# Kernel tuning notes

Measured on AMD Instinct MI355X. Metric: run time of the kernel, lower is better.

Reference implementation:

```python
import jax, jax.numpy as jnp
import numpy as np

B, T, D, H = 2, 2048, 512, 8
HD = D // H


def _mha(x, Wi, bi, Wo, bo):
    # torch nn.MultiheadAttention with q=k=v=x, eval mode (no dropout), batch-first math
    b, t, d = x.shape
    qkv = x @ Wi.T + bi                      # (b,t,3D)
    q, k, v = jnp.split(qkv, 3, axis=-1)
    q = q.reshape(b, t, H, HD)
    k = k.reshape(b, t, H, HD)
    v = v.reshape(b, t, H, HD)
    scores = jnp.einsum('bqhd,bkhd->bhqk', q, k) / jnp.sqrt(jnp.float32(HD))
    attn = jax.nn.softmax(scores, axis=-1)   # (b,H,t,t)
    out = jnp.einsum('bhqk,bkhd->bqhd', attn, v).reshape(b, t, d) @ Wo.T + bo
    return out, attn.mean(axis=1)            # weights averaged over heads, torch default


def _block_ids(t, c):
    # importance score is the constant c at every position (grad of sum == ones)
    cum = jnp.cumsum(jnp.full((t,), c, dtype=jnp.float32))
    frac = cum % 1.0
    boundary = (frac < jnp.roll(frac, 1)).astype(jnp.int32)
    return jnp.cumsum(boundary)              # ids in [0, max_blocks]


def _merge(x, ids, m):
    # segment-mean over dynamic blocks; block id 0 (pre-first-boundary) is dropped, as in torch loop i=1..max
    xm = jnp.moveaxis(x, 1, 0)               # (t,b,d)
    sums = jax.ops.segment_sum(xm, ids, num_segments=m + 1)[1:]              # (m,b,d)
    counts = jax.ops.segment_sum(jnp.ones(ids.shape[0], jnp.float32), ids, num_segments=m + 1)[1:]
    merged = sums / (counts[:, None, None] + 1e-10)
    return jnp.moveaxis(merged, 0, 1), counts


def setup_inputs():
    key = jax.random.key(0)
    ks = jax.random.split(key, 12)
    s = 0.02
    d = {'x': jax.random.normal(ks[0], (B, T, D), jnp.float32)}
    for i, n in enumerate(['char', 'block', 'glob']):
        d[n + '_Wi'] = jax.random.normal(ks[1 + 3 * i], (3 * D, D), jnp.float32) * s
        d[n + '_bi'] = jnp.zeros((3 * D,), jnp.float32)
        d[n + '_Wo'] = jax.random.normal(ks[2 + 3 * i], (D, D), jnp.float32) * s
        d[n + '_bo'] = jnp.zeros((D,), jnp.float32)
    d['merge_w'] = jax.random.normal(ks[10], (D,), jnp.float32) * 0.01
    d['merge_b'] = jnp.array([0.37], jnp.float32)
    d['gmerge_w'] = jax.random.normal(ks[11], (D,), jnp.float32) * 0.01
    d['gmerge_b'] = jnp.array([0.41], jnp.float32)
    return d


def reference(x, char_Wi, char_bi, char_Wo, char_bo, block_Wi, block_bi, block_Wo, block_bo,
              glob_Wi, glob_bi, glob_Wo, glob_bo, merge_w, merge_b, gmerge_w, gmerge_b):
    char_out, char_w = _mha(x, char_Wi, char_bi, char_Wo, char_bo)
    c1 = merge_w.sum() + merge_b[0]
    ids1 = _block_ids(T, c1)
    m1 = int(ids1.max())                      # data-independent given weights; concrete in eager
    blocks, cnt1 = _merge(char_out, ids1, m1)
    block_out, block_w = _mha(blocks, block_Wi, block_bi, block_Wo, block_bo)
    c2 = gmerge_w.sum() + gmerge_b[0]
    ids2 = _block_ids(m1, c2)
    m2 = int(ids2.max())
    glob, cnt2 = _merge(block_out, ids2, m2)
    glob_out, glob_w = _mha(glob, glob_Wi, glob_bi, glob_Wo, glob_bo)
    # double repeat_interleave expansion == gather: token t -> char block -> global block
    ids1n = np.asarray(ids1)
    ids2n = np.asarray(ids2)
    token_g = np.where(ids1n >= 1, ids2n[np.maximum(ids1n - 1, 0)], 0)
    tok_idx = np.nonzero(token_g >= 1)[0]
    expanded = glob_out[:, jnp.asarray(token_g[tok_idx] - 1), :]
    return expanded, char_w, block_w, glob_w
```

## Files before the change

kernel.cpp:

```cpp
#include <hip/hip_runtime.h>
#include <cstdint>
#include <cstddef>


#define TB 2
#define TT 2048
#define TD 512
#define TH 8
#define THD 64
#define KC 4

#define MI_M1 0
#define MI_M2 1
#define MI_NTOK 2
#define MI_OFF_CW 3
#define MI_OFF_BW 4
#define MI_OFF_GW 5
#define MI_MCHAR 6
#define MI_MBLOCK 7
#define MI_MGLOB 8
#define MI_SEQC 9
#define MI_SEQB 10
#define MI_SEQG 11

typedef _Float16 half8 __attribute__((ext_vector_type(8)));
typedef _Float16 half4 __attribute__((ext_vector_type(4)));
typedef _Float16 half2_t __attribute__((ext_vector_type(2)));
typedef float floatx4 __attribute__((ext_vector_type(4)));

__device__ __forceinline__ floatx4 mfma16(half8 a, half8 b, floatx4 c) {
  return __builtin_amdgcn_mfma_f32_16x16x32_f16(a, b, c, 0, 0, 0);
}
__device__ __forceinline__ floatx4 mfma16k16(half4 a, half4 b, floatx4 c) {
  return __builtin_amdgcn_mfma_f32_16x16x16f16(a, b, c, 0, 0, 0);
}

__device__ __forceinline__ void barrier_nodrain() {
  asm volatile("s_waitcnt lgkmcnt(0)" ::: "memory");
  __builtin_amdgcn_s_barrier();
}

__device__ __forceinline__ double fracd(double x) { return x - floor(x); }

__device__ int scan_phase(int n, double c, int* __restrict__ ids,
                          int* __restrict__ startg, float* __restrict__ cntg,
                          int* __restrict__ wsum, int t)
{
  int loc[8];
  const int base = t * 8;
#pragma unroll
  for (int j = 0; j < 8; ++j) {
    const int i = base + j;
    int f = 0;
    if (i < n) {
      const int pidx = (i == 0) ? n : i;
      f = (fracd((double)(i + 1) * c) < fracd((double)pidx * c)) ? 1 : 0;
    }
    loc[j] = f + ((j > 0) ? loc[j - 1] : 0);
  }
  wsum[t] = loc[7];
  __syncthreads();
  for (int off = 1; off < 256; off <<= 1) {
    int u = 0;
    if (t >= off) u = wsum[t - off];
    __syncthreads();
    wsum[t] += u;
    __syncthreads();
  }
  const int excl = wsum[t] - loc[7];
  const int m = wsum[255];
#pragma unroll
  for (int j = 0; j < 8; ++j) {
    const int i = base + j;
    if (i < n) {
      const int id = excl + loc[j];
      ids[i] = id;
      const int f = loc[j] - ((j > 0) ? loc[j - 1] : 0);
      if (f) startg[id - 1] = i;
    }
  }
  __syncthreads();
  for (int j = t; j < m; j += 256)
    cntg[j] = (float)((((j + 1) < m) ? startg[j + 1] : n) - startg[j]);
  __syncthreads();
  return m;
}

__global__ __launch_bounds__(256)
void meta_kernel(const float* __restrict__ mw, const float* __restrict__ mb,
                 const float* __restrict__ gw, const float* __restrict__ gb,
                 int* __restrict__ mi,
                 int* __restrict__ start1, float* __restrict__ cnt1,
                 int* __restrict__ start2, float* __restrict__ cnt2,
                 int* __restrict__ gmap)
{
  __shared__ int ids1[TT];
  __shared__ int ids2[TT];
  __shared__ int wsum[256];
  __shared__ double dsh[256];
  const int t = threadIdx.x;

  double s1 = 0.0, s2 = 0.0;
  for (int i = t; i < TD; i += 256) { s1 += (double)mw[i]; s2 += (double)gw[i]; }
  dsh[t] = s1; __syncthreads();
  for (int off = 128; off > 0; off >>= 1) {
    if (t < off) dsh[t] += dsh[t + off];
    __syncthreads();
  }
  const double c1 = dsh[0] + (double)mb[0];
  __syncthreads();
  dsh[t] = s2; __syncthreads();
  for (int off = 128; off > 0; off >>= 1) {
    if (t < off) dsh[t] += dsh[t + off];
    __syncthreads();
  }
  const double c2 = dsh[0] + (double)gb[0];
  __syncthreads();

  const int m1 = scan_phase(TT, c1, ids1, start1, cnt1, wsum, t);
  const int m2 = scan_phase(m1, c2, ids2, start2, cnt2, wsum, t);

  int i0 = TT;
  if (m1 >= 1 && m2 >= 1) i0 = start1[start2[0]];
  const int ntok = TT - i0;

  if (t == 0) {
    mi[MI_M1] = m1; mi[MI_M2] = m2; mi[MI_NTOK] = ntok;
    const int offcw = TB * ntok * TD;
    mi[MI_OFF_CW] = offcw;
    mi[MI_OFF_BW] = offcw + TB * TT * TT;
    mi[MI_OFF_GW] = offcw + TB * TT * TT + TB * m1 * m1;
    mi[MI_MCHAR] = TB * TT;
    mi[MI_MBLOCK] = TB * m1;
    mi[MI_MGLOB] = TB * m2;
    mi[MI_SEQC] = TT;
    mi[MI_SEQB] = m1;
    mi[MI_SEQG] = m2;
  }
  for (int i = i0 + t; i < TT; i += 256)
    gmap[i - i0] = ids2[ids1[i] - 1] - 1;
}

__global__ __launch_bounds__(256)
void prep_convert(const float* __restrict__ x,
                  const float* __restrict__ wi0, const float* __restrict__ wi1,
                  const float* __restrict__ wi2,
                  const float* __restrict__ wo0, const float* __restrict__ wo1,
                  const float* __restrict__ wo2,
                  _Float16* __restrict__ xh, _Float16* __restrict__ wiH,
                  _Float16* __restrict__ woH, _Float16* __restrict__ woL)
{
  const int r = blockIdx.y;
  const float* src;
  _Float16* dh;
  _Float16* dl = nullptr;
  int n;
  if (r == 0)      { src = x;   dh = xh;                              n = TB * TT * TD; }
  else if (r == 1) { src = wi0; dh = wiH;                             n = 3 * TD * TD; }
  else if (r == 2) { src = wi1; dh = wiH + (size_t)1 * 3 * TD * TD;   n = 3 * TD * TD; }
  else if (r == 3) { src = wi2; dh = wiH + (size_t)2 * 3 * TD * TD;   n = 3 * TD * TD; }
  else if (r == 4) { src = wo0; dh = woH; dl = woL;                   n = TD * TD; }
  else if (r == 5) { src = wo1; dh = woH + (size_t)TD * TD; dl = woL + (size_t)TD * TD; n = TD * TD; }
  else             { src = wo2; dh = woH + (size_t)2 * TD * TD; dl = woL + (size_t)2 * TD * TD; n = TD * TD; }

  const int stride = gridDim.x * 256 * 4;
  for (int i = (blockIdx.x * 256 + threadIdx.x) * 4; i < n; i += stride) {
    const float4 v = *(const float4*)&src[i];
    const float a[4] = {v.x, v.y, v.z, v.w};
    half4 h, l;
#pragma unroll
    for (int e = 0; e < 4; ++e) {
      const _Float16 hh = (_Float16)a[e];
      h[e] = hh;
      l[e] = (_Float16)(a[e] - (float)hh);
    }
    *(half4*)&dh[i] = h;
    if (dl) *(half4*)&dl[i] = l;
  }
}

__global__ __launch_bounds__(256)
void gemm_mfma(const _Float16* __restrict__ A, const _Float16* __restrict__ W,
               const float* __restrict__ bias, _Float16* __restrict__ C,
               const int* __restrict__ mi, int m_slot, int N)
{
  const int M = mi[m_slot];
  const int bm = blockIdx.y * 128;
  if (bm >= M) return;
  const int bn = blockIdx.x * 64;
  __shared__ _Float16 Ah[2][128][40];
  __shared__ _Float16 Wh[2][64][40];

  const int t = threadIdx.x;
  const int wv = t >> 6;
  const int lane = t & 63;
  const int l15 = lane & 15;
  const int quad = lane >> 4;
  const int srowA = t >> 1;
  const int ssegA = (t & 1) * 16;
  const int srowW = t >> 2;
  const int ssegW = (t & 3) * 8;
  const int ar = bm + srowA;
  const size_t abase = (size_t)ar * TD + ssegA;
  const size_t wbase = (size_t)(bn + srowW) * TD + ssegW;

  floatx4 acc[2][4];
#pragma unroll
  for (int i = 0; i < 2; ++i)
#pragma unroll
    for (int j = 0; j < 4; ++j) acc[i][j] = (floatx4){0.f, 0.f, 0.f, 0.f};

  const half8 h8z = {};
  half8 pa0, pa1, pw;

  auto LOADT = [&](int kk) {
    pa0 = h8z; pa1 = h8z;
    if (ar < M) {
      pa0 = *(const half8*)&A[abase + kk];
      pa1 = *(const half8*)&A[abase + kk + 8];
    }
    pw = *(const half8*)&W[wbase + kk];
  };
  auto WRITET = [&](int buf) {
    *(half8*)&Ah[buf][srowA][ssegA] = pa0;
    *(half8*)&Ah[buf][srowA][ssegA + 8] = pa1;
    *(half8*)&Wh[buf][srowW][ssegW] = pw;
  };

  LOADT(0);
  for (int it = 0; it < TD / 32; ++it) {
    const int buf = it & 1;
    WRITET(buf);
    if (it + 1 < TD / 32) LOADT((it + 1) * 32);
    barrier_nodrain();
    half8 ah[2];
#pragma unroll
    for (int mp = 0; mp < 2; ++mp)
      ah[mp] = *(const half8*)&Ah[buf][wv * 32 + mp * 16 + l15][quad * 8];
#pragma unroll
    for (int np = 0; np < 4; ++np) {
      const half8 bh = *(const half8*)&Wh[buf][np * 16 + l15][quad * 8];
#pragma unroll
      for (int mp = 0; mp < 2; ++mp)
        acc[mp][np] = mfma16(ah[mp], bh, acc[mp][np]);
    }
  }
  float bv[4];
#pragma unroll
  for (int np = 0; np < 4; ++np) bv[np] = bias[bn + np * 16 + l15];
#pragma unroll
  for (int mp = 0; mp < 2; ++mp) {
#pragma unroll
    for (int r = 0; r < 4; ++r) {
      const int row = bm + wv * 32 + mp * 16 + quad * 4 + r;
      if (row < M) {
        _Float16* cp = &C[(size_t)row * N + bn];
#pragma unroll
        for (int np = 0; np < 4; ++np)
          cp[np * 16 + l15] = (_Float16)(acc[mp][np][r] + bv[np]);
      }
    }
  }
}

__global__ __launch_bounds__(256)
void gemm_norm_mfma(const _Float16* __restrict__ Ob, const float* __restrict__ lb,
                    const _Float16* __restrict__ Whg, const _Float16* __restrict__ Wlg,
                    const float* __restrict__ bias,
                    float* __restrict__ C, const int* __restrict__ mi,
                    int m_slot, int seq_slot)
{
  const int M = mi[m_slot];
  const int bm = blockIdx.y * 64;
  if (bm >= M) return;
  const int seq = mi[seq_slot];
  const int bn = blockIdx.x * 64;
  __shared__ _Float16 Ah[2][64][40];
  __shared__ _Float16 Al[2][64][40];
  __shared__ _Float16 Wh[2][64][40];
  __shared__ _Float16 Wl[2][64][40];

  const int t = threadIdx.x;
  const int wv = t >> 6;
  const int lane = t & 63;
  const int l15 = lane & 15;
  const int quad = lane >> 4;
  const int srow = t >> 2;
  const int sseg = (t & 3) * 8;

  const int ar = bm + srow;
  const int ab = (ar >= seq) ? 1 : 0;
  const int aq = ar - ab * seq;
  const size_t wbase = (size_t)(bn + srow) * TD + sseg;

  floatx4 acc[4];
#pragma unroll
  for (int j = 0; j < 4; ++j) acc[j] = (floatx4){0.f, 0.f, 0.f, 0.f};

  const half8 h8z = {};
  half8 pOb[KC];
  float plb[KC];
  half8 pwh, pwl;

  auto LOADT = [&](int kk) {
    if (ar < M) {
      const size_t off = (size_t)ar * TD + kk + sseg;
#pragma unroll
      for (int z = 0; z < KC; ++z)
        pOb[z] = *(const half8*)&Ob[(size_t)z * 2097152 + off];
      const int h = kk >> 6;
      const size_t lidx = ((size_t)(ab * TH + h)) * 2048 + aq;
#pragma unroll
      for (int z = 0; z < KC; ++z) plb[z] = lb[(size_t)z * 32768 + lidx];
    } else {
#pragma unroll
      for (int z = 0; z < KC; ++z) { pOb[z] = h8z; plb[z] = 1.f; }
    }
    pwh = *(const half8*)&Whg[wbase + kk];
    pwl = *(const half8*)&Wlg[wbase + kk];
  };
  auto WRITET = [&](int buf) {
    float aa[8] = {0.f, 0.f, 0.f, 0.f, 0.f, 0.f, 0.f, 0.f};
    if (ar < M) {
#pragma unroll
      for (int z = 0; z < KC; ++z)
#pragma unroll
        for (int e = 0; e < 8; ++e) aa[e] += (float)pOb[z][e];
      const float lt = plb[0] + plb[1] + plb[2] + plb[3];
      const float linv = 1.f / lt;
#pragma unroll
      for (int e = 0; e < 8; ++e) aa[e] *= linv;
    }
    half8 hi, lo;
#pragma unroll
    for (int e = 0; e < 8; ++e) {
      const _Float16 h = (_Float16)aa[e];
      hi[e] = h; lo[e] = (_Float16)(aa[e] - (float)h);
    }
    *(half8*)&Ah[buf][srow][sseg] = hi;
    *(half8*)&Al[buf][srow][sseg] = lo;
    *(half8*)&Wh[buf][srow][sseg] = pwh;
    *(half8*)&Wl[buf][srow][sseg] = pwl;
  };

  LOADT(0);
  for (int it = 0; it < TD / 32; ++it) {
    const int buf = it & 1;
    WRITET(buf);
    if (it + 1 < TD / 32) LOADT((it + 1) * 32);
    barrier_nodrain();
    const half8 ah = *(const half8*)&Ah[buf][wv * 16 + l15][quad * 8];
    const half8 al = *(const half8*)&Al[buf][wv * 16 + l15][quad * 8];
#pragma unroll
    for (int np = 0; np < 4; ++np) {
      const half8 bh = *(const half8*)&Wh[buf][np * 16 + l15][quad * 8];
      const half8 bl = *(const half8*)&Wl[buf][np * 16 + l15][quad * 8];
      acc[np] = mfma16(al, bh, acc[np]);
      acc[np] = mfma16(ah, bl, acc[np]);
      acc[np] = mfma16(ah, bh, acc[np]);
    }
  }
  float bv[4];
#pragma unroll
  for (int np = 0; np < 4; ++np) bv[np] = bias[bn + np * 16 + l15];
#pragma unroll
  for (int r = 0; r < 4; ++r) {
    const int row = bm + wv * 16 + quad * 4 + r;
    if (row < M) {
      float* cp = &C[(size_t)row * 512 + bn];
#pragma unroll
      for (int np = 0; np < 4; ++np)
        cp[np * 16 + l15] = acc[np][r] + bv[np];
    }
  }
}

__global__ __launch_bounds__(256)
void attn1_mfma(const _Float16* __restrict__ qkv,
                float* __restrict__ lbase, _Float16* __restrict__ Obase,
                const int* __restrict__ mi, int seq_slot)
{
  const int seq = mi[seq_slot];
  const int q0 = blockIdx.x * 128;
  if (q0 >= seq) return;
  const int b = blockIdx.y >> 3, h = blockIdx.y & 7;
  const int z = blockIdx.z;
  float* lP = lbase + (size_t)z * 32768;
  _Float16* oP = Obase + (size_t)z * 2097152;
  const int t = threadIdx.x;
  const int wv = t >> 6;
  const int lane = t & 63;
  const int l15 = lane & 15;
  const int quad = lane >> 4;

  __shared__ __align__(16) char smem_raw[36864];
  float (*Ot)[68] = (float (*)[68])smem_raw;

  half8 qB[2][2];
#pragma unroll
  for (int mp = 0; mp < 2; ++mp) {
    const int qrow = q0 + wv * 32 + mp * 16 + l15;
#pragma unroll
    for (int c = 0; c < 2; ++c) {
      half8 v = {};
      if (qrow < seq)
        v = *(const half8*)&qkv[((size_t)(b * seq + qrow)) * 1536 + h * 64 + c * 32 + quad * 8];
      qB[mp][c] = v;
    }
  }
  half4 onesA;
#pragma unroll
  for (int j = 0; j < 4; ++j) onesA[j] = (_Float16)1.0f;

  floatx4 oacc[2][4];
#pragma unroll
  for (int i = 0; i < 2; ++i)
#pragma unroll
    for (int j = 0; j < 4; ++j) oacc[i][j] = (floatx4){0.f, 0.f, 0.f, 0.f};
  floatx4 lacc[2] = {(floatx4){0.f, 0.f, 0.f, 0.f}, (floatx4){0.f, 0.f, 0.f, 0.f}};

  const int nkt = (seq + 63) >> 6;
  const int nkc = (nkt + KC - 1) / KC;
  const int kt_beg = z * nkc;
  const int kt_end = min(kt_beg + nkc, nkt);

  const int krow = t >> 2;
  const int kseg = (t & 3) * 16;
  const int tp = lane & 31;
  const int dsel = lane >> 5;
  const int dbase = wv * 16 + dsel * 8;

  const half8 h8z = {};
  half8 pk0, pk1, pva, pvb;

  auto LOADKV = [&](int kt) {
    const int k0 = kt * 64;
    pk0 = h8z; pk1 = h8z; pva = h8z; pvb = h8z;
    const int kg = k0 + krow;
    if (kg < seq) {
      const _Float16* base = &qkv[((size_t)(b * seq + kg)) * 1536 + 512 + h * 64 + kseg];
      pk0 = *(const half8*)base;
      pk1 = *(const half8*)(base + 8);
    }
    const int kg0 = k0 + tp * 2;
    if (kg0 < seq)
      pva = *(const half8*)&qkv[((size_t)(b * seq + kg0)) * 1536 + 1024 + h * 64 + dbase];
    if (kg0 + 1 < seq)
      pvb = *(const half8*)&qkv[((size_t)(b * seq + kg0 + 1)) * 1536 + 1024 + h * 64 + dbase];
  };

  LOADKV(kt_beg);
  for (int kt = kt_beg; kt < kt_end; ++kt) {
    char* sb = smem_raw + (size_t)((kt - kt_beg) & 1) * 18432;
    _Float16 (*Kf)[72] = (_Float16 (*)[72])sb;
    _Float16 (*Vt)[72] = (_Float16 (*)[72])(sb + 9216);

    *(half8*)&Kf[krow][kseg] = pk0;
    *(half8*)&Kf[krow][kseg + 8] = pk1;
#pragma unroll
    for (int j = 0; j < 8; ++j) {
      half2_t pkk; pkk[0] = pva[j]; pkk[1] = pvb[j];
      *(half2_t*)&Vt[dbase + j][tp * 2] = pkk;
    }
    if (kt + 1 < kt_end) LOADKV(kt + 1);
    barrier_nodrain();

    const int k0 = kt * 64;
    const bool kfull = (k0 + 64 <= seq);
#pragma unroll
    for (int p = 0; p < 4; ++p) {
      floatx4 sT[2] = {(floatx4){0.f, 0.f, 0.f, 0.f}, (floatx4){0.f, 0.f, 0.f, 0.f}};
#pragma unroll
      for (int c = 0; c < 2; ++c) {
        const half8 kA = *(const half8*)&Kf[p * 16 + l15][c * 32 + quad * 8];
#pragma unroll
        for (int mp = 0; mp < 2; ++mp)
          sT[mp] = mfma16(kA, qB[mp][c], sT[mp]);
      }
      half4 vA[4];
#pragma unroll
      for (int dblk = 0; dblk < 4; ++dblk)
        vA[dblk] = *(const half4*)&Vt[dblk * 16 + l15][p * 16 + quad * 4];
      const int kg = k0 + p * 16 + quad * 4;
#pragma unroll
      for (int mp = 0; mp < 2; ++mp) {
        half4 eB;
        if (kfull) {
#pragma unroll
          for (int r = 0; r < 4; ++r)
            eB[r] = (_Float16)__expf(sT[mp][r] * 0.125f);
        } else {
#pragma unroll
          for (int r = 0; r < 4; ++r) {
            const float e = (kg + r < seq) ? __expf(sT[mp][r] * 0.125f) : 0.f;
            eB[r] = (_Float16)e;
          }
        }
        lacc[mp] = mfma16k16(onesA, eB, lacc[mp]);
#pragma unroll
        for (int dblk = 0; dblk < 4; ++dblk)
          oacc[mp][dblk] = mfma16k16(vA[dblk], eB, oacc[mp][dblk]);
      }
    }
  }

  __syncthreads();

#pragma unroll
  for (int mp = 0; mp < 2; ++mp) {
#pragma unroll
    for (int dblk = 0; dblk < 4; ++dblk)
      *(floatx4*)&Ot[wv * 16 + l15][dblk * 16 + quad * 4] = oacc[mp][dblk];
    const int ql = lane >> 2;
    const int dseg = (lane & 3) * 4;
    const int qg = q0 + wv * 32 + mp * 16 + ql;
    if (qg < seq) {
      _Float16* op = &oP[((size_t)(b * seq + qg)) * 512 + h * 64];
#pragma unroll
      for (int u = 0; u < 4; ++u) {
        const float4 v = *(const float4*)&Ot[wv * 16 + ql][u * 16 + dseg];
        half4 hv;
        hv[0] = (_Float16)v.x; hv[1] = (_Float16)v.y;
        hv[2] = (_Float16)v.z; hv[3] = (_Float16)v.w;
        *(half4*)(op + u * 16 + dseg) = hv;
      }
    }
    if (quad == 0) {
      const int qg2 = q0 + wv * 32 + mp * 16 + l15;
      if (qg2 < seq)
        lP[((size_t)(b * TH + h)) * 2048 + qg2] = lacc[mp][0];
    }
  }
}

__global__ __launch_bounds__(256)
void attn2_mfma(const _Float16* __restrict__ qkv,
                const float* __restrict__ lb,
                float* __restrict__ outb, const int* __restrict__ mi,
                int seq_slot, int off_slot)
{
  const int seq = mi[seq_slot];
  const int q0 = blockIdx.y * 64;
  const int k0 = blockIdx.x * 128;
  if (q0 >= seq || k0 >= seq) return;
  const int b = blockIdx.z;
  const int woff = mi[off_slot];
  float* wout = outb + (size_t)woff + (size_t)b * seq * seq;

  __shared__ _Float16 Ksh[2][128][72];
  __shared__ float Linv8[TH][64];

  const int t = threadIdx.x;
  const int wv = t >> 6;
  const int lane = t & 63;
  const int l15 = lane & 15;
  const int quad = lane >> 4;
  const int srowK = t >> 1;
  const int ssegK = (t & 1) * 32;

  for (int i = t; i < TH * 64; i += 256) {
    const int hh = i >> 6;
    const int qq = i & 63;
    float lv = 1.f;
    if (q0 + qq < seq) {
      const size_t lidx = ((size_t)(b * TH + hh)) * 2048 + q0 + qq;
      float lt = 0.f;
#pragma unroll
      for (int zz = 0; zz < KC; ++zz) lt += lb[(size_t)zz * 32768 + lidx];
      lv = lt;
    }
    Linv8[hh][qq] = 1.f / lv;
  }

  floatx4 acc[8];
#pragma unroll
  for (int j = 0; j < 8; ++j) acc[j] = (floatx4){0.f, 0.f, 0.f, 0.f};

  const int qr = q0 + wv * 16 + l15;
  const int kr = k0 + srowK;
  const bool qok = (qr < seq);
  const bool kok = (kr < seq);
  const size_t qoff = (size_t)(b * seq + qr) * 1536 + quad * 8;
  const size_t koff = (size_t)(b * seq + kr) * 1536 + 512 + ssegK;

  const half8 h8z = {};
  half8 pk[4];
  half8 qcur0, qcur1, qnxt0, qnxt1;

  auto LOADK = [&](int h) {
#pragma unroll
    for (int u = 0; u < 4; ++u) {
      pk[u] = h8z;
      if (kok) pk[u] = *(const half8*)&qkv[koff + h * 64 + u * 8];
    }
  };
  auto LOADQ = [&](int h, half8& d0, half8& d1) {
    d0 = h8z; d1 = h8z;
    if (qok) {
      d0 = *(const half8*)&qkv[qoff + h * 64];
      d1 = *(const half8*)&qkv[qoff + h * 64 + 32];
    }
  };

  LOADK(0);
  LOADQ(0, qcur0, qcur1);
  for (int h = 0; h < TH; ++h) {
    const int buf = h & 1;
#pragma unroll
    for (int u = 0; u < 4; ++u)
      *(half8*)&Ksh[buf][srowK][ssegK + u * 8] = pk[u];
    if (h + 1 < TH) { LOADK(h + 1); LOADQ(h + 1, qnxt0, qnxt1); }
    barrier_nodrain();

    float lv[4];
#pragma unroll
    for (int r = 0; r < 4; ++r)
      lv[r] = Linv8[h][wv * 16 + quad * 4 + r];

#pragma unroll
    for (int np = 0; np < 8; ++np) {
      const half8 bf0 = *(const half8*)&Ksh[buf][np * 16 + l15][quad * 8];
      const half8 bf1 = *(const half8*)&Ksh[buf][np * 16 + l15][32 + quad * 8];
      floatx4 s = (floatx4){0.f, 0.f, 0.f, 0.f};
      s = mfma16(qcur0, bf0, s);
      s = mfma16(qcur1, bf1, s);
#pragma unroll
      for (int r = 0; r < 4; ++r)
        acc[np][r] += __expf(s[r] * 0.125f) * lv[r];
    }
    qcur0 = qnxt0; qcur1 = qnxt1;
  }

#pragma unroll
  for (int r = 0; r < 4; ++r) {
    const int qg = q0 + wv * 16 + quad * 4 + r;
    if (qg >= seq) continue;
    float* rowp = wout + (size_t)qg * seq;
#pragma unroll
    for (int np = 0; np < 8; ++np) {
      const int col = k0 + np * 16 + l15;
      if (col < seq) rowp[col] = acc[np][r] * 0.125f;
    }
  }
}

__global__ __launch_bounds__(256)
void merge_kernel(const float* __restrict__ src, _Float16* __restrict__ dst,
                  const int* __restrict__ start, const float* __restrict__ cnt,
                  const int* __restrict__ mi, int seqin_slot, int seqout_slot)
{
  const int j = blockIdx.x;
  const int b = blockIdx.y;
  const int seqo = mi[seqout_slot];
  if (j >= seqo) return;
  const int seqi = mi[seqin_slot];
  const int s = start[j];
  const float cf = cnt[j];
  const int n = (int)cf;
  const int d0 = threadIdx.x * 2;
  float s0 = 0.f, s1 = 0.f;
  const float* p = &src[((size_t)b * seqi + s) * TD + d0];
  for (int i = 0; i < n; ++i) {
    const float2 v = *(const float2*)p;
    s0 += v.x; s1 += v.y;
    p += TD;
  }
  const float inv = 1.f / (cf + 1e-10f);
  half2_t o;
  o[0] = (_Float16)(s0 * inv);
  o[1] = (_Float16)(s1 * inv);
  *(half2_t*)&dst[((size_t)b * seqo + j) * TD + d0] = o;
}

__global__ __launch_bounds__(256)
void expand_kernel(const float* __restrict__ gout, float* __restrict__ dout,
                   const int* __restrict__ gmap, const int* __restrict__ mi)
{
  const int j = blockIdx.x;
  const int b = blockIdx.y;
  const int ntok = mi[MI_NTOK];
  if (j >= ntok) return;
  const int m2 = mi[MI_M2];
  const int g = gmap[j];
  const int d0 = threadIdx.x * 2;
  const float2 v = *(const float2*)&gout[((size_t)b * m2 + g) * TD + d0];
  *(float2*)&dout[((size_t)b * ntok + j) * TD + d0] = v;
}

extern "C" void kernel_launch(void* const* d_in, const int* in_sizes, int n_in,
                              void* d_out, int out_size, void* d_ws, size_t ws_size,
                              hipStream_t stream)
{
  const float* x   = (const float*)d_in[0];
  const float* cWi = (const float*)d_in[1];
  const float* cbi = (const float*)d_in[2];
  const float* cWo = (const float*)d_in[3];
  const float* cbo = (const float*)d_in[4];
  const float* bWi = (const float*)d_in[5];
  const float* bbi = (const float*)d_in[6];
  const float* bWo = (const float*)d_in[7];
  const float* bbo = (const float*)d_in[8];
  const float* gWi = (const float*)d_in[9];
  const float* gbi = (const float*)d_in[10];
  const float* gWo = (const float*)d_in[11];
  const float* gbo = (const float*)d_in[12];
  const float* mw  = (const float*)d_in[13];
  const float* mbv = (const float*)d_in[14];
  const float* gw  = (const float*)d_in[15];
  const float* gbv = (const float*)d_in[16];
  float* outf = (float*)d_out;

  char* wsb = (char*)d_ws;
  int*   mi     = (int*)(wsb);
  int*   start1 = (int*)(wsb + 1024);
  float* cnt1   = (float*)(wsb + 1024 + 8192);
  int*   start2 = (int*)(wsb + 1024 + 2 * 8192);
  float* cnt2   = (float*)(wsb + 1024 + 3 * 8192);
  int*   gmap   = (int*)(wsb + 1024 + 4 * 8192);
  float* lbase  = (float*)(wsb + 65536);
  _Float16* qkv = (_Float16*)(wsb + 655360);
  _Float16* Obase = (_Float16*)(wsb + 655360 + 12582912);
  float* stg_o  = (float*)(wsb + 30015488);
  _Float16* stg_mh = (_Float16*)(wsb + 38404096);
  _Float16* xh  = (_Float16*)(wsb + 42598400);
  _Float16* wiH = (_Float16*)(wsb + 46792704);
  _Float16* woH = (_Float16*)(wsb + 51511296);
  _Float16* woL = (_Float16*)(wsb + 53084160);

  const dim3 blk(256);

  meta_kernel<<<dim3(1), blk, 0, stream>>>(mw, mbv, gw, gbv, mi, start1, cnt1, start2, cnt2, gmap);
  prep_convert<<<dim3(256, 7), blk, 0, stream>>>(x, cWi, bWi, gWi, cWo, bWo, gWo,
                                                 xh, wiH, woH, woL);

  gemm_mfma<<<dim3(24, 32), blk, 0, stream>>>(xh, wiH, cbi, qkv, mi, MI_MCHAR, 1536);
  attn1_mfma<<<dim3(16, 16, KC), blk, 0, stream>>>(qkv, lbase, Obase, mi, MI_SEQC);
  attn2_mfma<<<dim3(16, 32, 2), blk, 0, stream>>>(qkv, lbase, outf, mi, MI_SEQC, MI_OFF_CW);
  gemm_norm_mfma<<<dim3(8, 64), blk, 0, stream>>>(Obase, lbase, woH, woL, cbo, stg_o, mi, MI_MCHAR, MI_SEQC);
  merge_kernel<<<dim3(2048, 2), blk, 0, stream>>>(stg_o, stg_mh, start1, cnt1, mi, MI_SEQC, MI_SEQB);

  gemm_mfma<<<dim3(24, 32), blk, 0, stream>>>(stg_mh, wiH + (size_t)786432, bbi, qkv, mi, MI_MBLOCK, 1536);
  attn1_mfma<<<dim3(16, 16, KC), blk, 0, stream>>>(qkv, lbase, Obase, mi, MI_SEQB);
  attn2_mfma<<<dim3(16, 32, 2), blk, 0, stream>>>(qkv, lbase, outf, mi, MI_SEQB, MI_OFF_BW);
  gemm_norm_mfma<<<dim3(8, 64), blk, 0, stream>>>(Obase, lbase, woH + (size_t)262144, woL + (size_t)262144, bbo, stg_o, mi, MI_MBLOCK, MI_SEQB);
  merge_kernel<<<dim3(2048, 2), blk, 0, stream>>>(stg_o, stg_mh, start2, cnt2, mi, MI_SEQB, MI_SEQG);

  gemm_mfma<<<dim3(24, 32), blk, 0, stream>>>(stg_mh, wiH + (size_t)2 * 786432, gbi, qkv, mi, MI_MGLOB, 1536);
  attn1_mfma<<<dim3(16, 16, KC), blk, 0, stream>>>(qkv, lbase, Obase, mi, MI_SEQG);
  attn2_mfma<<<dim3(16, 32, 2), blk, 0, stream>>>(qkv, lbase, outf, mi, MI_SEQG, MI_OFF_GW);
  gemm_norm_mfma<<<dim3(8, 64), blk, 0, stream>>>(Obase, lbase, woH + (size_t)2 * 262144, woL + (size_t)2 * 262144, gbo, stg_o, mi, MI_MGLOB, MI_SEQG);
  expand_kernel<<<dim3(2048, 2), blk, 0, stream>>>(stg_o, outf, gmap, mi);

  (void)in_sizes; (void)n_in; (void)out_size; (void)ws_size;
}
```

Measured before the change: 332.8 us.

## Fuse meta and prep kernels; double query tile in both attention passes

Merges the single-block metadata scan into the weight/input fp16 conversion launch as an extra grid row, saving one launch and letting the scan overlap the conversion. Doubles the query rows per block in attn1 (128 to 256) and attn2 (64 to 128), so each loaded K/V tile is reused across more queries with fewer blocks launched. The larger per-thread accumulators raise register pressure and halve the block count, which can lower occupancy and parallelism for the short block/global sequences.

```diff
diff --git a/kernel.cpp b/kernel.cpp
--- a/kernel.cpp
+++ b/kernel.cpp
@@ -87,12 +87,19 @@
 }
 
 __global__ __launch_bounds__(256)
-void meta_kernel(const float* __restrict__ mw, const float* __restrict__ mb,
-                 const float* __restrict__ gw, const float* __restrict__ gb,
-                 int* __restrict__ mi,
-                 int* __restrict__ start1, float* __restrict__ cnt1,
-                 int* __restrict__ start2, float* __restrict__ cnt2,
-                 int* __restrict__ gmap)
+void meta_prep(const float* __restrict__ mw, const float* __restrict__ mb,
+               const float* __restrict__ gw, const float* __restrict__ gb,
+               int* __restrict__ mi,
+               int* __restrict__ start1, float* __restrict__ cnt1,
+               int* __restrict__ start2, float* __restrict__ cnt2,
+               int* __restrict__ gmap,
+               const float* __restrict__ x,
+               const float* __restrict__ wi0, const float* __restrict__ wi1,
+               const float* __restrict__ wi2,
+               const float* __restrict__ wo0, const float* __restrict__ wo1,
+               const float* __restrict__ wo2,
+               _Float16* __restrict__ xh, _Float16* __restrict__ wiH,
+               _Float16* __restrict__ woH, _Float16* __restrict__ woL)
 {
   __shared__ int ids1[TT];
   __shared__ int ids2[TT];
@@ -100,56 +107,50 @@
   __shared__ double dsh[256];
   const int t = threadIdx.x;
 
-  double s1 = 0.0, s2 = 0.0;
-  for (int i = t; i < TD; i += 256) { s1 += (double)mw[i]; s2 += (double)gw[i]; }
-  dsh[t] = s1; __syncthreads();
-  for (int off = 128; off > 0; off >>= 1) {
-    if (t < off) dsh[t] += dsh[t + off];
+  if (blockIdx.y == 7) {
+    if (blockIdx.x != 0) return;
+    double s1 = 0.0, s2 = 0.0;
+    for (int i = t; i < TD; i += 256) { s1 += (double)mw[i]; s2 += (double)gw[i]; }
+    dsh[t] = s1; __syncthreads();
+    for (int off = 128; off > 0; off >>= 1) {
+      if (t < off) dsh[t] += dsh[t + off];
+      __syncthreads();
+    }
+    const double c1 = dsh[0] + (double)mb[0];
     __syncthreads();
-  }
-  const double c1 = dsh[0] + (double)mb[0];
-  __syncthreads();
-  dsh[t] = s2; __syncthreads();
-  for (int off = 128; off > 0; off >>= 1) {
-    if (t < off) dsh[t] += dsh[t + off];
+    dsh[t] = s2; __syncthreads();
+    for (int off = 128; off > 0; off >>= 1) {
+      if (t < off) dsh[t] += dsh[t + off];
+      __syncthreads();
+    }
+    const double c2 = dsh[0] + (double)gb[0];
     __syncthreads();
-  }
-  const double c2 = dsh[0] + (double)gb[0];
-  __syncthreads();
-
-  const int m1 = scan_phase(TT, c1, ids1, start1, cnt1, wsum, t);
-  const int m2 = scan_phase(m1, c2, ids2, start2, cnt2, wsum, t);
-
-  int i0 = TT;
-  if (m1 >= 1 && m2 >= 1) i0 = start1[start2[0]];
-  const int ntok = TT - i0;
-
-  if (t == 0) {
-    mi[MI_M1] = m1; mi[MI_M2] = m2; mi[MI_NTOK] = ntok;
-    const int offcw = TB * ntok * TD;
-    mi[MI_OFF_CW] = offcw;
-    mi[MI_OFF_BW] = offcw + TB * TT * TT;
-    mi[MI_OFF_GW] = offcw + TB * TT * TT + TB * m1 * m1;
-    mi[MI_MCHAR] = TB * TT;
-    mi[MI_MBLOCK] = TB * m1;
-    mi[MI_MGLOB] = TB * m2;
-    mi[MI_SEQC] = TT;
-    mi[MI_SEQB] = m1;
-    mi[MI_SEQG] = m2;
-  }
-  for (int i = i0 + t; i < TT; i += 256)
-    gmap[i - i0] = ids2[ids1[i] - 1] - 1;
-}
-
-__global__ __launch_bounds__(256)
-void prep_convert(const float* __restrict__ x,
-                  const float* __restrict__ wi0, const float* __restrict__ wi1,
-                  const float* __restrict__ wi2,
-                  const float* __restrict__ wo0, const float* __restrict__ wo1,
-                  const float* __restrict__ wo2,
-                  _Float16* __restrict__ xh, _Float16* __restrict__ wiH,
-                  _Float16* __restrict__ woH, _Float16* __restrict__ woL)
-{
+
+    const int m1 = scan_phase(TT, c1, ids1, start1, cnt1, wsum, t);
+    const int m2 = scan_phase(m1, c2, ids2, start2, cnt2, wsum, t);
+
+    int i0 = TT;
+    if (m1 >= 1 && m2 >= 1) i0 = start1[start2[0]];
+    const int ntok = TT - i0;
+
+    if (t == 0) {
+      mi[MI_M1] = m1; mi[MI_M2] = m2; mi[MI_NTOK] = ntok;
+      const int offcw = TB * ntok * TD;
+      mi[MI_OFF_CW] = offcw;
+      mi[MI_OFF_BW] = offcw + TB * TT * TT;
+      mi[MI_OFF_GW] = offcw + TB * TT * TT + TB * m1 * m1;
+      mi[MI_MCHAR] = TB * TT;
+      mi[MI_MBLOCK] = TB * m1;
+      mi[MI_MGLOB] = TB * m2;
+      mi[MI_SEQC] = TT;
+      mi[MI_SEQB] = m1;
+      mi[MI_SEQG] = m2;
+    }
+    for (int i = i0 + t; i < TT; i += 256)
+      gmap[i - i0] = ids2[ids1[i] - 1] - 1;
+    return;
+  }
+
   const int r = blockIdx.y;
   const float* src;
   _Float16* dh;
@@ -381,7 +382,7 @@
                 const int* __restrict__ mi, int seq_slot)
 {
   const int seq = mi[seq_slot];
-  const int q0 = blockIdx.x * 128;
+  const int q0 = blockIdx.x * 256;
   if (q0 >= seq) return;
   const int b = blockIdx.y >> 3, h = blockIdx.y & 7;
   const int z = blockIdx.z;
@@ -396,10 +397,10 @@
   __shared__ __align__(16) char smem_raw[36864];
   float (*Ot)[68] = (float (*)[68])smem_raw;
 
-  half8 qB[2][2];
-#pragma unroll
-  for (int mp = 0; mp < 2; ++mp) {
-    const int qrow = q0 + wv * 32 + mp * 16 + l15;
+  half8 qB[4][2];
+#pragma unroll
+  for (int mp = 0; mp < 4; ++mp) {
+    const int qrow = q0 + wv * 64 + mp * 16 + l15;
 #pragma unroll
     for (int c = 0; c < 2; ++c) {
       half8 v = {};
@@ -412,12 +413,14 @@
 #pragma unroll
   for (int j = 0; j < 4; ++j) onesA[j] = (_Float16)1.0f;
 
-  floatx4 oacc[2][4];
-#pragma unroll
-  for (int i = 0; i < 2; ++i)
+  floatx4 oacc[4][4];
+#pragma unroll
+  for (int i = 0; i < 4; ++i)
 #pragma unroll
     for (int j = 0; j < 4; ++j) oacc[i][j] = (floatx4){0.f, 0.f, 0.f, 0.f};
-  floatx4 lacc[2] = {(floatx4){0.f, 0.f, 0.f, 0.f}, (floatx4){0.f, 0.f, 0.f, 0.f}};
+  floatx4 lacc[4];
+#pragma unroll
+  for (int i = 0; i < 4; ++i) lacc[i] = (floatx4){0.f, 0.f, 0.f, 0.f};
 
   const int nkt = (seq + 63) >> 6;
   const int nkc = (nkt + KC - 1) / KC;
@@ -469,12 +472,14 @@
     const bool kfull = (k0 + 64 <= seq);
 #pragma unroll
     for (int p = 0; p < 4; ++p) {
-      floatx4 sT[2] = {(floatx4){0.f, 0.f, 0.f, 0.f}, (floatx4){0.f, 0.f, 0.f, 0.f}};
+      floatx4 sT[4];
+#pragma unroll
+      for (int mp = 0; mp < 4; ++mp) sT[mp] = (floatx4){0.f, 0.f, 0.f, 0.f};
 #pragma unroll
       for (int c = 0; c < 2; ++c) {
         const half8 kA = *(const half8*)&Kf[p * 16 + l15][c * 32 + quad * 8];
 #pragma unroll
-        for (int mp = 0; mp < 2; ++mp)
+        for (int mp = 0; mp < 4; ++mp)
           sT[mp] = mfma16(kA, qB[mp][c], sT[mp]);
       }
       half4 vA[4];
@@ -483,7 +488,7 @@
         vA[dblk] = *(const half4*)&Vt[dblk * 16 + l15][p * 16 + quad * 4];
       const int kg = k0 + p * 16 + quad * 4;
 #pragma unroll
-      for (int mp = 0; mp < 2; ++mp) {
+      for (int mp = 0; mp < 4; ++mp) {
         half4 eB;
         if (kfull) {
 #pragma unroll
@@ -507,13 +512,13 @@
   __syncthreads();
 
 #pragma unroll
-  for (int mp = 0; mp < 2; ++mp) {
+  for (int mp = 0; mp < 4; ++mp) {
 #pragma unroll
     for (int dblk = 0; dblk < 4; ++dblk)
       *(floatx4*)&Ot[wv * 16 + l15][dblk * 16 + quad * 4] = oacc[mp][dblk];
     const int ql = lane >> 2;
     const int dseg = (lane & 3) * 4;
-    const int qg = q0 + wv * 32 + mp * 16 + ql;
+    const int qg = q0 + wv * 64 + mp * 16 + ql;
     if (qg < seq) {
       _Float16* op = &oP[((size_t)(b * seq + qg)) * 512 + h * 64];
 #pragma unroll
@@ -526,7 +531,7 @@
       }
     }
     if (quad == 0) {
-      const int qg2 = q0 + wv * 32 + mp * 16 + l15;
+      const int qg2 = q0 + wv * 64 + mp * 16 + l15;
       if (qg2 < seq)
         lP[((size_t)(b * TH + h)) * 2048 + qg2] = lacc[mp][0];
     }
@@ -540,7 +545,7 @@
                 int seq_slot, int off_slot)
 {
   const int seq = mi[seq_slot];
-  const int q0 = blockIdx.y * 64;
+  const int q0 = blockIdx.y * 128;
   const int k0 = blockIdx.x * 128;
   if (q0 >= seq || k0 >= seq) return;
   const int b = blockIdx.z;
@@ -548,7 +553,7 @@
   float* wout = outb + (size_t)woff + (size_t)b * seq * seq;
 
   __shared__ _Float16 Ksh[2][128][72];
-  __shared__ float Linv8[TH][64];
+  __shared__ float Linv8[TH][128];
 
   const int t = threadIdx.x;
   const int wv = t >> 6;
@@ -558,9 +563,9 @@
   const int srowK = t >> 1;
   const int ssegK = (t & 1) * 32;
 
-  for (int i = t; i < TH * 64; i += 256) {
-    const int hh = i >> 6;
-    const int qq = i & 63;
+  for (int i = t; i < TH * 128; i += 256) {
+    const int hh = i >> 7;
+    const int qq = i & 127;
     float lv = 1.f;
     if (q0 + qq < seq) {
       const size_t lidx = ((size_t)(b * TH + hh)) * 2048 + q0 + qq;
@@ -572,20 +577,27 @@
     Linv8[hh][qq] = 1.f / lv;
   }
 
-  floatx4 acc[8];
-#pragma unroll
-  for (int j = 0; j < 8; ++j) acc[j] = (floatx4){0.f, 0.f, 0.f, 0.f};
-
-  const int qr = q0 + wv * 16 + l15;
+  floatx4 acc[2][8];
+#pragma unroll
+  for (int mp = 0; mp < 2; ++mp)
+#pragma unroll
+    for (int j = 0; j < 8; ++j) acc[mp][j] = (floatx4){0.f, 0.f, 0.f, 0.f};
+
   const int kr = k0 + srowK;
-  const bool qok = (qr < seq);
   const bool kok = (kr < seq);
-  const size_t qoff = (size_t)(b * seq + qr) * 1536 + quad * 8;
   const size_t koff = (size_t)(b * seq + kr) * 1536 + 512 + ssegK;
+
+  int qr[2]; bool qok[2]; size_t qoff[2];
+#pragma unroll
+  for (int mp = 0; mp < 2; ++mp) {
+    qr[mp] = q0 + wv * 32 + mp * 16 + l15;
+    qok[mp] = (qr[mp] < seq);
+    qoff[mp] = (size_t)(b * seq + qr[mp]) * 1536 + quad * 8;
+  }
 
   const half8 h8z = {};
   half8 pk[4];
-  half8 qcur0, qcur1, qnxt0, qnxt1;
+  half8 qcur[2][2], qnxt[2][2];
 
   auto LOADK = [&](int h) {
 #pragma unroll
@@ -594,52 +606,67 @@
       if (kok) pk[u] = *(const half8*)&qkv[koff + h * 64 + u * 8];
     }
   };
-  auto LOADQ = [&](int h, half8& d0, half8& d1) {
-    d0 = h8z; d1 = h8z;
-    if (qok) {
-      d0 = *(const half8*)&qkv[qoff + h * 64];
-      d1 = *(const half8*)&qkv[qoff + h * 64 + 32];
+  auto LOADQ = [&](int h, half8 (&d)[2][2]) {
+#pragma unroll
+    for (int mp = 0; mp < 2; ++mp) {
+      d[mp][0] = h8z; d[mp][1] = h8z;
+      if (qok[mp]) {
+        d[mp][0] = *(const half8*)&qkv[qoff[mp] + h * 64];
+        d[mp][1] = *(const half8*)&qkv[qoff[mp] + h * 64 + 32];
+      }
     }
   };
 
   LOADK(0);
-  LOADQ(0, qcur0, qcur1);
+  LOADQ(0, qcur);
   for (int h = 0; h < TH; ++h) {
     const int buf = h & 1;
 #pragma unroll
     for (int u = 0; u < 4; ++u)
       *(half8*)&Ksh[buf][srowK][ssegK + u * 8] = pk[u];
-    if (h + 1 < TH) { LOADK(h + 1); LOADQ(h + 1, qnxt0, qnxt1); }
+    if (h + 1 < TH) { LOADK(h + 1); LOADQ(h + 1, qnxt); }
     barrier_nodrain();
 
-    float lv[4];
-#pragma unroll
-    for (int r = 0; r < 4; ++r)
-      lv[r] = Linv8[h][wv * 16 + quad * 4 + r];
+    float lv[2][4];
+#pragma unroll
+    for (int mp = 0; mp < 2; ++mp)
+#pragma unroll
+      for (int r = 0; r < 4; ++r)
+        lv[mp][r] = Linv8[h][wv * 32 + mp * 16 + quad * 4 + r];
 
 #pragma unroll
     for (int np = 0; np < 8; ++np) {
       const half8 bf0 = *(const half8*)&Ksh[buf][np * 16 + l15][quad * 8];
       const half8 bf1 = *(const half8*)&Ksh[buf][np * 16 + l15][32 + quad * 8];
-      floatx4 s = (floatx4){0.f, 0.f, 0.f, 0.f};
-      s = mfma16(qcur0, bf0, s);
-      s = mfma16(qcur1, bf1, s);
-#pragma unroll
-      for (int r = 0; r < 4; ++r)
-        acc[np][r] += __expf(s[r] * 0.125f) * lv[r];
-    }
-    qcur0 = qnxt0; qcur1 = qnxt1;
-  }
-
-#pragma unroll
-  for (int r = 0; r < 4; ++r) {
-    const int qg = q0 + wv * 16 + quad * 4 + r;
-    if (qg >= seq) continue;
-    float* rowp = wout + (size_t)qg * seq;
-#pragma unroll
-    for (int np = 0; np < 8; ++np) {
-      const int col = k0 + np * 16 + l15;
-      if (col < seq) rowp[col] = acc[np][r] * 0.125f;
+#pragma unroll
+      for (int mp = 0; mp < 2; ++mp) {
+        floatx4 s = (floatx4){0.f, 0.f, 0.f, 0.f};
+        s = mfma16(qcur[mp][0], bf0, s);
+        s = mfma16(qcur[mp][1], bf1, s);
+#pragma unroll
+        for (int r = 0; r < 4; ++r)
+          acc[mp][np][r] += __expf(s[r] * 0.125f) * lv[mp][r];
+      }
+    }
+#pragma unroll
+    for (int mp = 0; mp < 2; ++mp) {
+      qcur[mp][0] = qnxt[mp][0];
+      qcur[mp][1] = qnxt[mp][1];
+    }
+  }
+
+#pragma unroll
+  for (int mp = 0; mp < 2; ++mp) {
+#pragma unroll
+    for (int r = 0; r < 4; ++r) {
+      const int qg = q0 + wv * 32 + mp * 16 + quad * 4 + r;
+      if (qg >= seq) continue;
+      float* rowp = wout + (size_t)qg * seq;
+#pragma unroll
+      for (int np = 0; np < 8; ++np) {
+        const int col = k0 + np * 16 + l15;
+        if (col < seq) rowp[col] = acc[mp][np][r] * 0.125f;
+      }
     }
   }
 }
@@ -729,25 +756,26 @@
 
   const dim3 blk(256);
 
-  meta_kernel<<<dim3(1), blk, 0, stream>>>(mw, mbv, gw, gbv, mi, start1, cnt1, start2, cnt2, gmap);
-  prep_convert<<<dim3(256, 7), blk, 0, stream>>>(x, cWi, bWi, gWi, cWo, bWo, gWo,
-                                                 xh, wiH, woH, woL);
+  meta_prep<<<dim3(256, 8), blk, 0, stream>>>(mw, mbv, gw, gbv, mi, start1, cnt1,
+                                              start2, cnt2, gmap,
+                                              x, cWi, bWi, gWi, cWo, bWo, gWo,
+                                              xh, wiH, woH, woL);
 
   gemm_mfma<<<dim3(24, 32), blk, 0, stream>>>(xh, wiH, cbi, qkv, mi, MI_MCHAR, 1536);
-  attn1_mfma<<<dim3(16, 16, KC), blk, 0, stream>>>(qkv, lbase, Obase, mi, MI_SEQC);
-  attn2_mfma<<<dim3(16, 32, 2), blk, 0, stream>>>(qkv, lbase, outf, mi, MI_SEQC, MI_OFF_CW);
+  attn1_mfma<<<dim3(8, 16, KC), blk, 0, stream>>>(qkv, lbase, Obase, mi, MI_SEQC);
+  attn2_mfma<<<dim3(16, 16, 2), blk, 0, stream>>>(qkv, lbase, outf, mi, MI_SEQC, MI_OFF_CW);
   gemm_norm_mfma<<<dim3(8, 64), blk, 0, stream>>>(Obase, lbase, woH, woL, cbo, stg_o, mi, MI_MCHAR, MI_SEQC);
   merge_kernel<<<dim3(2048, 2), blk, 0, stream>>>(stg_o, stg_mh, start1, cnt1, mi, MI_SEQC, MI_SEQB);
 
   gemm_mfma<<<dim3(24, 32), blk, 0, stream>>>(stg_mh, wiH + (size_t)786432, bbi, qkv, mi, MI_MBLOCK, 1536);
-  attn1_mfma<<<dim3(16, 16, KC), blk, 0, stream>>>(qkv, lbase, Obase, mi, MI_SEQB);
-  attn2_mfma<<<dim3(16, 32, 2), blk, 0, stream>>>(qkv, lbase, outf, mi, MI_SEQB, MI_OFF_BW);
+  attn1_mfma<<<dim3(8, 16, KC), blk, 0, stream>>>(qkv, lbase, Obase, mi, MI_SEQB);
+  attn2_mfma<<<dim3(16, 16, 2), blk, 0, stream>>>(qkv, lbase, outf, mi, MI_SEQB, MI_OFF_BW);
   gemm_norm_mfma<<<dim3(8, 64), blk, 0, stream>>>(Obase, lbase, woH + (size_t)262144, woL + (size_t)262144, bbo, stg_o, mi, MI_MBLOCK, MI_SEQB);
   merge_kernel<<<dim3(2048, 2), blk, 0, stream>>>(stg_o, stg_mh, start2, cnt2, mi, MI_SEQB, MI_SEQG);
 
   gemm_mfma<<<dim3(24, 32), blk, 0, stream>>>(stg_mh, wiH + (size_t)2 * 786432, gbi, qkv, mi, MI_MGLOB, 1536);
-  attn1_mfma<<<dim3(16, 16, KC), blk, 0, stream>>>(qkv, lbase, Obase, mi, MI_SEQG);
-  attn2_mfma<<<dim3(16, 32, 2), blk, 0, stream>>>(qkv, lbase, outf, mi, MI_SEQG, MI_OFF_GW);
+  attn1_mfma<<<dim3(8, 16, KC), blk, 0, stream>>>(qkv, lbase, Obase, mi, MI_SEQG);
+  attn2_mfma<<<dim3(16, 16, 2), blk, 0, stream>>>(qkv, lbase, outf, mi, MI_SEQG, MI_OFF_GW);
   gemm_norm_mfma<<<dim3(8, 64), blk, 0, stream>>>(Obase, lbase, woH + (size_t)2 * 262144, woL + (size_t)2 * 262144, gbo, stg_o, mi, MI_MGLOB, MI_SEQG);
   expand_kernel<<<dim3(2048, 2), blk, 0, stream>>>(stg_o, outf, gmap, mi);
 
```

After: 372.3 us. 1.12x slower.
